# Performance work log

Measured on AMD Instinct MI355X. Metric: run time of the kernel, lower is better.

The kernel has to match this reference:

```python
import jax, jax.numpy as jnp
import numpy as np

H = 16   # n_heads == n_I
D = 64   # d_q = d_k = d_v = d_r
DX = H * D
B, S = 4, 2048

def setup_inputs() -> dict:
    key = jax.random.key(0)
    ks = jax.random.split(key, 9)
    sc = 0.02
    return {
        "value": jax.random.normal(ks[0], (B, S, DX), jnp.float32),
        "key":   jax.random.normal(ks[1], (B, S, DX), jnp.float32),
        "query": jax.random.normal(ks[2], (B, S, DX), jnp.float32),
        "Wq_w": jax.random.normal(ks[3], (DX, DX), jnp.float32) * sc,
        "Wq_b": jnp.zeros((DX,), jnp.float32),
        "Wk_w": jax.random.normal(ks[4], (DX, DX), jnp.float32) * sc,
        "Wk_b": jnp.zeros((DX,), jnp.float32),
        "Wv_w": jax.random.normal(ks[5], (DX, DX), jnp.float32) * sc,
        "Wv_b": jnp.zeros((DX,), jnp.float32),
        "Wr_w": jax.random.normal(ks[6], (DX, DX), jnp.float32) * sc,
        "Wr_b": jnp.zeros((DX,), jnp.float32),
        "Wout_w": jax.random.normal(ks[7], (DX, DX), jnp.float32) * sc,
        "Wout_b": jnp.zeros((DX,), jnp.float32),
    }

def _heads(x, b, s):
    # [b, s, H*D] -> [b, H, s, D]
    return x.reshape(b, s, H, D).transpose(0, 2, 1, 3)

def reference(value, key, query, Wq_w, Wq_b, Wk_w, Wk_b, Wv_w, Wv_b,
              Wr_w, Wr_b, Wout_w, Wout_b):
    b, s, _ = query.shape
    # torch nn.Linear: y = x @ W.T + b
    Q = _heads(query @ Wq_w.T + Wq_b, b, s)   # [b,H,s,D]
    K = _heads(key   @ Wk_w.T + Wk_b, b, s)
    V = _heads(value @ Wv_w.T + Wv_b, b, s)
    R = _heads(query @ Wr_w.T + Wr_b, b, s)
    dot_scale = jnp.sqrt(jnp.float32(D))
    scores = jnp.einsum("bhid,bhjd->bhij", Q, K) / dot_scale  # [b,H,s,s]
    attn = jax.nn.softmax(scores, axis=-1)                    # dropout p=0
    out = jnp.einsum("bhij,bhjd->bhid", attn, V)              # [b,H,s,D]
    out = out * R                                             # R-gating
    out = out.transpose(0, 2, 1, 3).reshape(b, s, H * D)
    return out @ Wout_w.T + Wout_b
```

## Files before the change

### kernel.cpp

```cpp
#include <hip/hip_runtime.h>
#include <hip/hip_bf16.h>

typedef __bf16 bf16;
typedef __bf16 bf16x4 __attribute__((ext_vector_type(4)));
typedef __bf16 bf16x8 __attribute__((ext_vector_type(8)));
typedef float  f32x4  __attribute__((ext_vector_type(4)));

#define MFMA_16x16x32(a, b, c) __builtin_amdgcn_mfma_f32_16x16x32_bf16((a), (b), (c), 0, 0, 0)

typedef const void __attribute__((address_space(1))) gvoid;
typedef void __attribute__((address_space(3))) svoid;

__device__ __forceinline__ void async_copy16(const void* gptr, void* ldsptr) {
    __builtin_amdgcn_global_load_lds((gvoid*)gptr, (svoid*)ldsptr, 16, 0, 0);
}

__global__ void cvt3_acts(const float* __restrict__ s0, const float* __restrict__ s1,
                          const float* __restrict__ s2,
                          bf16* __restrict__ d0, bf16* __restrict__ d1, bf16* __restrict__ d2)
{
    constexpr int N4SEG = 8192 * 1024 / 4;
    int i = blockIdx.x * blockDim.x + threadIdx.x;
    const int stride = gridDim.x * blockDim.x;
    for (; i < 3 * N4SEG; i += stride) {
        const int seg = i / N4SEG;
        const int j = i - seg * N4SEG;
        const float* s = seg == 0 ? s0 : (seg == 1 ? s1 : s2);
        bf16* d = seg == 0 ? d0 : (seg == 1 ? d1 : d2);
        float4 v = ((const float4*)s)[j];
        bf16x4 o = { (bf16)v.x, (bf16)v.y, (bf16)v.z, (bf16)v.w };
        ((bf16x4*)d)[j] = o;
    }
}

__global__ void cvt5_wts(const float* __restrict__ s0, const float* __restrict__ s1,
                         const float* __restrict__ s2, const float* __restrict__ s3,
                         const float* __restrict__ s4,
                         bf16* __restrict__ d0, bf16* __restrict__ d1, bf16* __restrict__ d2,
                         bf16* __restrict__ d3, bf16* __restrict__ d4)
{
    constexpr int N4SEG = 1024 * 1024 / 4;
    int i = blockIdx.x * blockDim.x + threadIdx.x;
    const int stride = gridDim.x * blockDim.x;
    for (; i < 5 * N4SEG; i += stride) {
        const int seg = i / N4SEG;
        const int j = i - seg * N4SEG;
        const float* s = seg == 0 ? s0 : seg == 1 ? s1 : seg == 2 ? s2 : seg == 3 ? s3 : s4;
        bf16* d = seg == 0 ? d0 : seg == 1 ? d1 : seg == 2 ? d2 : seg == 3 ? d3 : d4;
        float4 v = ((const float4*)s)[j];
        bf16x4 o = { (bf16)v.x, (bf16)v.y, (bf16)v.z, (bf16)v.w };
        ((bf16x4*)d)[j] = o;
    }
}

template <typename OutT, bool TRANS>
__global__ void gemm_nt_bias(const bf16* __restrict__ X, const bf16* __restrict__ W,
                             const float* __restrict__ bias, OutT* __restrict__ Y,
                             int M, int N, int K)
{
    constexpr int SDIM = 2048;
    __shared__ alignas(16) bf16 As[128 * 32];
    __shared__ alignas(16) bf16 Bs[128 * 32];

    const int tid  = threadIdx.x;
    const int lane = tid & 63;
    const int wave = tid >> 6;
    const int wm   = wave >> 1;
    const int wn   = wave & 1;
    const int bm   = blockIdx.x * 128;
    const int bn   = blockIdx.y * 128;
    const int l15  = lane & 15;
    const int quad = lane >> 4;

    const int srow = lane >> 2;
    const int scol = (lane & 3) * 8;

    const bf16* aseg0 = X + (size_t)(bm + wave * 32 + srow) * K + scol;
    const bf16* aseg1 = X + (size_t)(bm + wave * 32 + 16 + srow) * K + scol;
    const bf16* bseg0 = W + (size_t)(bn + wave * 32 + srow) * K + scol;
    const bf16* bseg1 = W + (size_t)(bn + wave * 32 + 16 + srow) * K + scol;
    bf16* as0 = As + (wave * 2 + 0) * 512;
    bf16* as1 = As + (wave * 2 + 1) * 512;
    bf16* bs0 = Bs + (wave * 2 + 0) * 512;
    bf16* bs1 = Bs + (wave * 2 + 1) * 512;

    f32x4 acc[4][4] = {};

    for (int k0 = 0; k0 < K; k0 += 32) {
        __syncthreads();
        async_copy16(aseg0 + k0, as0);
        async_copy16(aseg1 + k0, as1);
        async_copy16(bseg0 + k0, bs0);
        async_copy16(bseg1 + k0, bs1);
        __syncthreads();

        bf16x8 af[4], bfr[4];
        #pragma unroll
        for (int i = 0; i < 4; ++i)
            af[i] = *(const bf16x8*)(As + (wm * 64 + i * 16 + l15) * 32 + quad * 8);
        #pragma unroll
        for (int j = 0; j < 4; ++j)
            bfr[j] = *(const bf16x8*)(Bs + (wn * 64 + j * 16 + l15) * 32 + quad * 8);
        #pragma unroll
        for (int i = 0; i < 4; ++i)
            #pragma unroll
            for (int j = 0; j < 4; ++j)
                acc[i][j] = MFMA_16x16x32(af[i], bfr[j], acc[i][j]);
    }

    #pragma unroll
    for (int i = 0; i < 4; ++i) {
        const int rowg = bm + wm * 64 + i * 16 + quad * 4;
        #pragma unroll
        for (int j = 0; j < 4; ++j) {
            const int colg = bn + wn * 64 + j * 16 + l15;
            const float bv = bias[colg];
            if (TRANS) {
                bf16x4 o;
                #pragma unroll
                for (int r = 0; r < 4; ++r) o[r] = (bf16)(acc[i][j][r] + bv);
                *(bf16x4*)((bf16*)Y + (size_t)(rowg >> 11) * N * SDIM
                                    + (size_t)colg * SDIM + (rowg & (SDIM - 1))) = o;
            } else {
                #pragma unroll
                for (int r = 0; r < 4; ++r)
                    Y[(size_t)(rowg + r) * N + colg] = (OutT)(acc[i][j][r] + bv);
            }
        }
    }
}

__launch_bounds__(256, 4)
__global__ void attn_fused(const bf16* __restrict__ QRp, const bf16* __restrict__ Kp,
                           const bf16* __restrict__ Vtp, bf16* __restrict__ Op)
{
    constexpr int S = 2048, DXc = 1024, QRST = 2048, Dh = 64;
    constexpr int PST = 88;
    __shared__ alignas(16) bf16 KsLo[64 * 32], KsHi[64 * 32];
    __shared__ alignas(16) bf16 VtLo[64 * 32], VtHi[64 * 32];
    __shared__ alignas(16) bf16 Pw[4][2][16 * PST];

    const int tid  = threadIdx.x;
    const int lane = tid & 63;
    const int wave = tid >> 6;
    const int qt = blockIdx.x, h = blockIdx.y, b = blockIdx.z;
    const int l15  = lane & 15;
    const int quad = lane >> 4;

    const size_t qrbase = ((size_t)b * S) * QRST + h * Dh;
    const size_t kbase  = ((size_t)b * S) * DXc + h * Dh;
    const size_t vtbase = ((size_t)(b * 16 + h) * Dh) * S;
    const size_t obase  = ((size_t)b * S) * DXc + h * Dh;

    constexpr float QSCALE = 0.125f * 1.44269504088896340736f;
    bf16x8 qf[2][2];
    #pragma unroll
    for (int mi = 0; mi < 2; ++mi) {
        const int qrow = qt * 128 + wave * 32 + mi * 16 + l15;
        const bf16* qptr = QRp + qrbase + (size_t)qrow * QRST + quad * 8;
        qf[mi][0] = *(const bf16x8*)(qptr);
        qf[mi][1] = *(const bf16x8*)(qptr + 32);
        #pragma unroll
        for (int j = 0; j < 8; ++j) {
            qf[mi][0][j] = (bf16)((float)qf[mi][0][j] * QSCALE);
            qf[mi][1][j] = (bf16)((float)qf[mi][1][j] * QSCALE);
        }
    }

    bf16x8 onesf;
    #pragma unroll
    for (int j = 0; j < 8; ++j) onesf[j] = (bf16)1.0f;

    f32x4 oacc[2][4] = {};
    f32x4 lacc[2] = {};

    const int srow = lane >> 2;
    const int scol = (lane & 3) * 8;
    const bf16* kseg = Kp  + kbase  + (size_t)(16 * wave + srow) * DXc + scol;
    const bf16* vseg = Vtp + vtbase + (size_t)(16 * wave + srow) * S   + scol;
    bf16* ksl = KsLo + wave * 512;
    bf16* ksh = KsHi + wave * 512;
    bf16* vtl = VtLo + wave * 512;
    bf16* vth = VtHi + wave * 512;

    for (int kv0 = 0; kv0 < S; kv0 += 64) {
        __syncthreads();
        async_copy16(kseg + (size_t)kv0 * DXc,      ksl);
        async_copy16(kseg + (size_t)kv0 * DXc + 32, ksh);
        async_copy16(vseg + kv0,                    vtl);
        async_copy16(vseg + kv0 + 32,               vth);
        __syncthreads();

        {
            bf16x8 kf[4][2];
            #pragma unroll
            for (int nb = 0; nb < 4; ++nb) {
                kf[nb][0] = *(const bf16x8*)(KsLo + (nb * 16 + l15) * 32 + quad * 8);
                kf[nb][1] = *(const bf16x8*)(KsHi + (nb * 16 + l15) * 32 + quad * 8);
            }
            #pragma unroll
            for (int mi = 0; mi < 2; ++mi) {
                f32x4 sacc[4];
                #pragma unroll
                for (int nb = 0; nb < 4; ++nb) {
                    f32x4 z = {0.f, 0.f, 0.f, 0.f};
                    z = MFMA_16x16x32(qf[mi][1], kf[nb][1], z);
                    sacc[nb] = MFMA_16x16x32(qf[mi][0], kf[nb][0], z);
                }
                bf16* pw = &Pw[wave][mi][0];
                #pragma unroll
                for (int nb = 0; nb < 4; ++nb) {
                    #pragma unroll
                    for (int r = 0; r < 4; ++r) {
                        float p = __builtin_exp2f(sacc[nb][r]);
                        pw[(quad * 4 + r) * PST + nb * 16 + l15] = (bf16)p;
                    }
                }
            }
        }

        {
            bf16x8 vf[4][2];
            #pragma unroll
            for (int nb = 0; nb < 4; ++nb) {
                vf[nb][0] = *(const bf16x8*)(VtLo + (nb * 16 + l15) * 32 + quad * 8);
                vf[nb][1] = *(const bf16x8*)(VtHi + (nb * 16 + l15) * 32 + quad * 8);
            }
            #pragma unroll
            for (int mi = 0; mi < 2; ++mi) {
                const bf16* pw = &Pw[wave][mi][0];
                bf16x8 pf0 = *(const bf16x8*)(pw + l15 * PST + quad * 8);
                bf16x8 pf1 = *(const bf16x8*)(pw + l15 * PST + 32 + quad * 8);
                lacc[mi] = MFMA_16x16x32(pf0, onesf, lacc[mi]);
                lacc[mi] = MFMA_16x16x32(pf1, onesf, lacc[mi]);
                #pragma unroll
                for (int db = 0; db < 4; ++db) {
                    oacc[mi][db] = MFMA_16x16x32(pf0, vf[db][0], oacc[mi][db]);
                    oacc[mi][db] = MFMA_16x16x32(pf1, vf[db][1], oacc[mi][db]);
                }
            }
        }
    }

    #pragma unroll
    for (int mi = 0; mi < 2; ++mi) {
        #pragma unroll
        for (int r = 0; r < 4; ++r) {
            const float inv = 1.0f / lacc[mi][r];
            const int row = qt * 128 + wave * 32 + mi * 16 + quad * 4 + r;
            const bf16* rrow = QRp + qrbase + (size_t)row * QRST + 1024;
            bf16* orow = Op + obase + (size_t)row * DXc;
            #pragma unroll
            for (int db = 0; db < 4; ++db) {
                const int d = db * 16 + l15;
                const float o = oacc[mi][db][r] * inv;
                const float rg = (float)rrow[d];
                orow[d] = (bf16)(o * rg);
            }
        }
    }
}

extern "C" void kernel_launch(void* const* d_in, const int* in_sizes, int n_in,
                              void* d_out, int out_size, void* d_ws, size_t ws_size,
                              hipStream_t stream)
{
    (void)in_sizes; (void)n_in; (void)out_size; (void)ws_size;
    constexpr int B = 4, S = 2048, DX = 1024, M = B * S;
    constexpr size_t MD = (size_t)M * DX;
    constexpr size_t WD = (size_t)DX * DX;

    const float* value  = (const float*)d_in[0];
    const float* keyi   = (const float*)d_in[1];
    const float* query  = (const float*)d_in[2];
    const float* Wq_w   = (const float*)d_in[3];
    const float* Wq_b   = (const float*)d_in[4];
    const float* Wk_w   = (const float*)d_in[5];
    const float* Wk_b   = (const float*)d_in[6];
    const float* Wv_w   = (const float*)d_in[7];
    const float* Wv_b   = (const float*)d_in[8];
    const float* Wr_w   = (const float*)d_in[9];
    const float* Wr_b   = (const float*)d_in[10];
    const float* Wout_w = (const float*)d_in[11];
    const float* Wout_b = (const float*)d_in[12];

    bf16* p = (bf16*)d_ws;
    bf16* xv  = p;  p += MD;
    bf16* xk  = p;  p += MD;
    bf16* xq  = p;  p += MD;
    bf16* wqr = p;  p += 2 * WD;
    bf16* wk  = p;  p += WD;
    bf16* wv  = p;  p += WD;
    bf16* wo  = p;  p += WD;
    bf16* qr  = p;  p += 2 * MD;
    bf16* kws = p;  p += MD;
    bf16* vtws= p;  p += MD;
    float* qrb = (float*)p;
    bf16* ows = xv;

    hipMemcpyAsync(qrb,        Wq_b, DX * sizeof(float), hipMemcpyDeviceToDevice, stream);
    hipMemcpyAsync(qrb + DX,   Wr_b, DX * sizeof(float), hipMemcpyDeviceToDevice, stream);

    cvt3_acts<<<dim3(2048), dim3(256), 0, stream>>>(value, keyi, query, xv, xk, xq);
    cvt5_wts <<<dim3(1024), dim3(256), 0, stream>>>(Wq_w, Wr_w, Wk_w, Wv_w, Wout_w,
                                                    wqr, wqr + WD, wk, wv, wo);

    dim3 gblk(256);
    gemm_nt_bias<bf16, false><<<dim3(M / 128, 2048 / 128), gblk, 0, stream>>>(
        xq, wqr, qrb, qr, M, 2048, DX);
    gemm_nt_bias<bf16, false><<<dim3(M / 128, DX / 128), gblk, 0, stream>>>(
        xk, wk, Wk_b, kws, M, DX, DX);
    gemm_nt_bias<bf16, true ><<<dim3(M / 128, DX / 128), gblk, 0, stream>>>(
        xv, wv, Wv_b, vtws, M, DX, DX);

    attn_fused<<<dim3(S / 128, 16, B), gblk, 0, stream>>>(qr, kws, vtws, ows);

    gemm_nt_bias<float, false><<<dim3(M / 128, DX / 128), gblk, 0, stream>>>(
        ows, wo, Wout_b, (float*)d_out, M, DX, DX);
}
```

Baseline: 405.1 us.

## Keep softmax probabilities in registers via transposed S^T MFMA layout

The attention loop now computes S^T (K as A operand, Q as B operand), so the exp2 outputs land directly in the register layout needed as the B operand of a 16x16x16 MFMA against V^T. This removes the per-wave LDS round trip for P and the extra MFMAs against a ones vector used for row sums. Row sums are kept as per-lane scalars and reduced with shuffles at the end, and the epilogue writes vectorized bf16x4 instead of scalar stores. The trade-off is more, smaller MFMAs (16x16x16 instead of 16x16x32) and changed V^T fragment loads.

```diff
diff --git a/kernel.cpp b/kernel.cpp
--- a/kernel.cpp
+++ b/kernel.cpp
@@ -4,9 +4,20 @@
 typedef __bf16 bf16;
 typedef __bf16 bf16x4 __attribute__((ext_vector_type(4)));
 typedef __bf16 bf16x8 __attribute__((ext_vector_type(8)));
+typedef short  s16x4  __attribute__((ext_vector_type(4)));
 typedef float  f32x4  __attribute__((ext_vector_type(4)));
 
 #define MFMA_16x16x32(a, b, c) __builtin_amdgcn_mfma_f32_16x16x32_bf16((a), (b), (c), 0, 0, 0)
+
+__device__ __forceinline__ f32x4 MFMA16x16x16(bf16x4 a, bf16x4 b, f32x4 c) {
+#if __has_builtin(__builtin_amdgcn_mfma_f32_16x16x16_bf16)
+    return __builtin_amdgcn_mfma_f32_16x16x16_bf16(a, b, c, 0, 0, 0);
+#else
+    union U { bf16x4 h; s16x4 s; };
+    U ua, ub; ua.h = a; ub.h = b;
+    return __builtin_amdgcn_mfma_f32_16x16x16bf16_1k(ua.s, ub.s, c, 0, 0, 0);
+#endif
+}
 
 typedef const void __attribute__((address_space(1))) gvoid;
 typedef void __attribute__((address_space(3))) svoid;
@@ -135,10 +146,8 @@
                            const bf16* __restrict__ Vtp, bf16* __restrict__ Op)
 {
     constexpr int S = 2048, DXc = 1024, QRST = 2048, Dh = 64;
-    constexpr int PST = 88;
     __shared__ alignas(16) bf16 KsLo[64 * 32], KsHi[64 * 32];
     __shared__ alignas(16) bf16 VtLo[64 * 32], VtHi[64 * 32];
-    __shared__ alignas(16) bf16 Pw[4][2][16 * PST];
 
     const int tid  = threadIdx.x;
     const int lane = tid & 63;
@@ -167,12 +176,8 @@
         }
     }
 
-    bf16x8 onesf;
-    #pragma unroll
-    for (int j = 0; j < 8; ++j) onesf[j] = (bf16)1.0f;
-
     f32x4 oacc[2][4] = {};
-    f32x4 lacc[2] = {};
+    float lsum[2] = {0.f, 0.f};
 
     const int srow = lane >> 2;
     const int scol = (lane & 3) * 8;
@@ -191,72 +196,56 @@
         async_copy16(vseg + kv0 + 32,               vth);
         __syncthreads();
 
-        {
-            bf16x8 kf[4][2];
+        #pragma unroll
+        for (int nb = 0; nb < 4; ++nb) {
+            bf16x8 kf0 = *(const bf16x8*)(KsLo + (nb * 16 + l15) * 32 + quad * 8);
+            bf16x8 kf1 = *(const bf16x8*)(KsHi + (nb * 16 + l15) * 32 + quad * 8);
+            const bf16* vbase = (nb < 2) ? VtLo : VtHi;
+            const int vcol = (nb & 1) * 16 + quad * 4;
+            bf16x4 vtf[4];
             #pragma unroll
-            for (int nb = 0; nb < 4; ++nb) {
-                kf[nb][0] = *(const bf16x8*)(KsLo + (nb * 16 + l15) * 32 + quad * 8);
-                kf[nb][1] = *(const bf16x8*)(KsHi + (nb * 16 + l15) * 32 + quad * 8);
-            }
+            for (int db = 0; db < 4; ++db)
+                vtf[db] = *(const bf16x4*)(vbase + (db * 16 + l15) * 32 + vcol);
+
             #pragma unroll
             for (int mi = 0; mi < 2; ++mi) {
-                f32x4 sacc[4];
+                f32x4 z = {0.f, 0.f, 0.f, 0.f};
+                z = MFMA_16x16x32(kf1, qf[mi][1], z);
+                z = MFMA_16x16x32(kf0, qf[mi][0], z);
+                bf16x4 pt;
                 #pragma unroll
-                for (int nb = 0; nb < 4; ++nb) {
-                    f32x4 z = {0.f, 0.f, 0.f, 0.f};
-                    z = MFMA_16x16x32(qf[mi][1], kf[nb][1], z);
-                    sacc[nb] = MFMA_16x16x32(qf[mi][0], kf[nb][0], z);
+                for (int r = 0; r < 4; ++r) {
+                    float p = __builtin_exp2f(z[r]);
+                    lsum[mi] += p;
+                    pt[r] = (bf16)p;
                 }
-                bf16* pw = &Pw[wave][mi][0];
                 #pragma unroll
-                for (int nb = 0; nb < 4; ++nb) {
-                    #pragma unroll
-                    for (int r = 0; r < 4; ++r) {
-                        float p = __builtin_exp2f(sacc[nb][r]);
-                        pw[(quad * 4 + r) * PST + nb * 16 + l15] = (bf16)p;
-                    }
-                }
+                for (int db = 0; db < 4; ++db)
+                    oacc[mi][db] = MFMA16x16x16(vtf[db], pt, oacc[mi][db]);
             }
         }
-
-        {
-            bf16x8 vf[4][2];
-            #pragma unroll
-            for (int nb = 0; nb < 4; ++nb) {
-                vf[nb][0] = *(const bf16x8*)(VtLo + (nb * 16 + l15) * 32 + quad * 8);
-                vf[nb][1] = *(const bf16x8*)(VtHi + (nb * 16 + l15) * 32 + quad * 8);
-            }
-            #pragma unroll
-            for (int mi = 0; mi < 2; ++mi) {
-                const bf16* pw = &Pw[wave][mi][0];
-                bf16x8 pf0 = *(const bf16x8*)(pw + l15 * PST + quad * 8);
-                bf16x8 pf1 = *(const bf16x8*)(pw + l15 * PST + 32 + quad * 8);
-                lacc[mi] = MFMA_16x16x32(pf0, onesf, lacc[mi]);
-                lacc[mi] = MFMA_16x16x32(pf1, onesf, lacc[mi]);
-                #pragma unroll
-                for (int db = 0; db < 4; ++db) {
-                    oacc[mi][db] = MFMA_16x16x32(pf0, vf[db][0], oacc[mi][db]);
-                    oacc[mi][db] = MFMA_16x16x32(pf1, vf[db][1], oacc[mi][db]);
-                }
-            }
-        }
     }
 
     #pragma unroll
     for (int mi = 0; mi < 2; ++mi) {
-        #pragma unroll
-        for (int r = 0; r < 4; ++r) {
-            const float inv = 1.0f / lacc[mi][r];
-            const int row = qt * 128 + wave * 32 + mi * 16 + quad * 4 + r;
-            const bf16* rrow = QRp + qrbase + (size_t)row * QRST + 1024;
-            bf16* orow = Op + obase + (size_t)row * DXc;
+        lsum[mi] += __shfl_xor(lsum[mi], 16, 64);
+        lsum[mi] += __shfl_xor(lsum[mi], 32, 64);
+    }
+
+    #pragma unroll
+    for (int mi = 0; mi < 2; ++mi) {
+        const float inv = 1.0f / lsum[mi];
+        const int qrow = qt * 128 + wave * 32 + mi * 16 + l15;
+        const bf16* rrow = QRp + qrbase + (size_t)qrow * QRST + 1024;
+        bf16* orow = Op + obase + (size_t)qrow * DXc;
+        #pragma unroll
+        for (int db = 0; db < 4; ++db) {
+            bf16x4 rg = *(const bf16x4*)(rrow + db * 16 + quad * 4);
+            bf16x4 o;
             #pragma unroll
-            for (int db = 0; db < 4; ++db) {
-                const int d = db * 16 + l15;
-                const float o = oacc[mi][db][r] * inv;
-                const float rg = (float)rrow[d];
-                orow[d] = (bf16)(o * rg);
-            }
+            for (int r = 0; r < 4; ++r)
+                o[r] = (bf16)(oacc[mi][db][r] * inv * (float)rg[r]);
+            *(bf16x4*)(orow + db * 16 + quad * 4) = o;
         }
     }
 }
@@ -298,8 +287,8 @@
     float* qrb = (float*)p;
     bf16* ows = xv;
 
-    hipMemcpyAsync(qrb,        Wq_b, DX * sizeof(float), hipMemcpyDeviceToDevice, stream);
-    hipMemcpyAsync(qrb + DX,   Wr_b, DX * sizeof(float), hipMemcpyDeviceToDevice, stream);
+    hipMemcpyAsync(qrb,      Wq_b, DX * sizeof(float), hipMemcpyDeviceToDevice, stream);
+    hipMemcpyAsync(qrb + DX, Wr_b, DX * sizeof(float), hipMemcpyDeviceToDevice, stream);
 
     cvt3_acts<<<dim3(2048), dim3(256), 0, stream>>>(value, keyi, query, xv, xk, xq);
     cvt5_wts <<<dim3(1024), dim3(256), 0, stream>>>(Wq_w, Wr_w, Wk_w, Wv_w, Wout_w,
```

After: 443.9 us. +9.6%, slower.
